# Kernel tuning notes

Measured on AMD Instinct MI355X. Metric: run time of the kernel, lower is better.

## Reference

```python
import jax, jax.numpy as jnp
import numpy as np
import math

B, T, C, D = 8, 2048, 1024, 1024
N_LAYER, LAYER_ID = 24, 12


def setup_inputs() -> dict:
    key = jax.random.key(0)
    ks = jax.random.split(key, 5)
    r01 = LAYER_ID / (N_LAYER - 1)
    r10 = 1.0 - LAYER_ID / N_LAYER
    ddd = np.arange(C, dtype=np.float64) / C                      # (C,)
    h = np.arange(D, dtype=np.float64)
    decay_speed = -5 + 8 * (h / (D - 1)) ** (0.7 + 1.3 * r01)     # time_decay init
    zigzag = ((np.arange(D) + 1) % 3 - 1) * 0.5
    time_first = np.log(0.3) + zigzag
    scale = C ** -0.5
    return {
        "x": jax.random.normal(ks[0], (B, T, C), jnp.float32),
        "time_decay": jnp.asarray(decay_speed, jnp.float32),
        "time_first": jnp.asarray(time_first, jnp.float32),
        "time_mix_k": jnp.asarray(ddd ** r10, jnp.float32),
        "time_mix_v": jnp.asarray(ddd ** r10 + 0.3 * r01, jnp.float32),
        "time_mix_r": jnp.asarray(ddd ** (0.5 * r10), jnp.float32),
        "Wk": jax.random.normal(ks[1], (D, C), jnp.float32) * scale,
        "Wv": jax.random.normal(ks[2], (D, C), jnp.float32) * scale,
        "Wr": jax.random.normal(ks[3], (D, C), jnp.float32) * scale,
        "Wo": jax.random.normal(ks[4], (C, D), jnp.float32) * scale,
    }


def _wkv(time_decay, time_first, k, v):
    # wkv_t = (e^{u+k_t} v_t + A_{t-1}) / (e^{u+k_t} + B_{t-1})
    # A_t = e^w A_{t-1} + e^{k_t} v_t ;  B_t likewise with v=1 ;  w = -exp(time_decay)
    # Exactly the math of the original conv1d-with-exp-curve trick, in O(T).
    ew = jnp.exp(-jnp.exp(time_decay))   # (D,)
    eu = jnp.exp(time_first)             # (D,)
    ek = jnp.exp(k)                      # [B,T,D]
    ekv = ek * v

    def step(carry, inp):
        a, b = carry                     # [B,D] each
        ekt, ekvt = inp                  # [B,D] each
        out = (eu * ekvt + a) / (eu * ekt + b)
        return (ew * a + ekvt, ew * b + ekt), out

    init = (jnp.zeros_like(ek[:, 0]), jnp.zeros_like(ek[:, 0]))
    xs = (jnp.swapaxes(ek, 0, 1), jnp.swapaxes(ekv, 0, 1))  # [T,B,D]
    _, out = jax.lax.scan(step, init, xs)
    return jnp.swapaxes(out, 0, 1)       # [B,T,D]


def reference(x, time_decay, time_first, time_mix_k, time_mix_v, time_mix_r, Wk, Wv, Wr, Wo):
    # time_shift: prepend zero row, drop last (ZeroPad2d((0,0,1,-1)))
    xx = jnp.pad(x, ((0, 0), (1, 0), (0, 0)))[:, :-1]
    xk = x * time_mix_k + xx * (1 - time_mix_k)
    xv = x * time_mix_v + xx * (1 - time_mix_v)
    xr = x * time_mix_r + xx * (1 - time_mix_r)
    k = jnp.einsum('btc,dc->btd', xk, Wk)
    v = jnp.einsum('btc,dc->btd', xv, Wv)
    sr = jax.nn.sigmoid(jnp.einsum('btc,dc->btd', xr, Wr))
    rwkv = sr * _wkv(time_decay, time_first, k, v)
    return jnp.einsum('btd,cd->btc', rwkv, Wo)
```

## Files before the change

### kernel.cpp

```cpp
#include <hip/hip_runtime.h>
#include <cstdint>
#include <cstddef>

#define Bb 8
#define Tt 2048
#define Cc 1024
#define Dd 1024
#define Mm (Bb*Tt)
#define CL 64
#define NCH (Tt/CL)


typedef __bf16  bf16x8  __attribute__((ext_vector_type(8)));
typedef float   floatx4 __attribute__((ext_vector_type(4)));

__device__ __forceinline__ ushort f2bf(float f) {
    unsigned u = __float_as_uint(f);
    u = (u + 0x7FFF + ((u >> 16) & 1)) >> 16;
    return (ushort)u;
}
__device__ __forceinline__ float bf2f(ushort u) {
    return __uint_as_float(((unsigned)u) << 16);
}

__device__ __forceinline__ void load_lds16(const void* g, void* l) {
    __builtin_amdgcn_global_load_lds((__attribute__((address_space(1))) void*)(g),
                                     (__attribute__((address_space(3))) void*)(l),
                                     16, 0, 0);
}

__global__ __launch_bounds__(256) void prep_mix(
        const float* __restrict__ x, const float* __restrict__ w,
        ushort* __restrict__ xm) {
    int i  = blockIdx.x * 256 + threadIdx.x;
    int cq = i & (Cc / 8 - 1);
    int m  = i >> 7;
    int t  = m & (Tt - 1);
    float4 xc0 = ((const float4*)x)[i * 2];
    float4 xc1 = ((const float4*)x)[i * 2 + 1];
    float4 xp0 = make_float4(0.f, 0.f, 0.f, 0.f);
    float4 xp1 = xp0;
    if (t != 0) {
        xp0 = ((const float4*)x)[(i - Cc / 8) * 2];
        xp1 = ((const float4*)x)[(i - Cc / 8) * 2 + 1];
    }
    float4 w0 = ((const float4*)w)[cq * 2];
    float4 w1 = ((const float4*)w)[cq * 2 + 1];
    ushort o[8];
    o[0] = f2bf(xc0.x * w0.x + xp0.x * (1.f - w0.x));
    o[1] = f2bf(xc0.y * w0.y + xp0.y * (1.f - w0.y));
    o[2] = f2bf(xc0.z * w0.z + xp0.z * (1.f - w0.z));
    o[3] = f2bf(xc0.w * w0.w + xp0.w * (1.f - w0.w));
    o[4] = f2bf(xc1.x * w1.x + xp1.x * (1.f - w1.x));
    o[5] = f2bf(xc1.y * w1.y + xp1.y * (1.f - w1.y));
    o[6] = f2bf(xc1.z * w1.z + xp1.z * (1.f - w1.z));
    o[7] = f2bf(xc1.w * w1.w + xp1.w * (1.f - w1.w));
    ((ulonglong2*)xm)[i] = *(const ulonglong2*)o;
}

__global__ __launch_bounds__(256) void cvt_w(
        const float* __restrict__ wk, const float* __restrict__ wv,
        const float* __restrict__ wr, const float* __restrict__ wo,
        ushort* __restrict__ ok, ushort* __restrict__ ov,
        ushort* __restrict__ orr, ushort* __restrict__ oo) {
    int i = blockIdx.x * 256 + threadIdx.x;
    int sel = i >> 18;
    int j = i & ((1 << 18) - 1);
    const float* s = sel == 0 ? wk : sel == 1 ? wv : sel == 2 ? wr : wo;
    ushort* d      = sel == 0 ? ok : sel == 1 ? ov : sel == 2 ? orr : oo;
    float4 f = ((const float4*)s)[j];
    ushort4 o;
    o.x = f2bf(f.x); o.y = f2bf(f.y); o.z = f2bf(f.z); o.w = f2bf(f.w);
    ((ushort4*)d)[j] = o;
}

template<int MODE>
__global__ __launch_bounds__(256) void gemm_nt(
        const ushort* __restrict__ A, const ushort* __restrict__ Bw,
        void* __restrict__ Co, int Ndim, int Kdim) {
    __shared__ __attribute__((aligned(16))) __bf16 As[128 * 32];
    __shared__ __attribute__((aligned(16))) __bf16 Bs[128 * 32];
    const int tid  = threadIdx.x;
    const int lane = tid & 63;
    const int quad = lane >> 4;
    const int fr   = lane & 15;
    const int wave = tid >> 6;
    const int wm   = (wave >> 1) * 64;
    const int wn   = (wave & 1) * 64;
    const long tm  = (long)blockIdx.x * 128;
    const long tn  = (long)blockIdx.y * 128;

    const int srow  = tid >> 2;
    const int spart = tid & 3;
    const ushort* Ag0 = A + (tm + srow) * (long)Kdim + spart * 8;
    const ushort* Ag1 = Ag0 + 64 * (long)Kdim;
    const ushort* Bg0 = Bw + (tn + srow) * (long)Kdim + spart * 8;
    const ushort* Bg1 = Bg0 + 64 * (long)Kdim;
    __bf16* AlA = &As[wave * 512];
    __bf16* AlB = &As[2048 + wave * 512];
    __bf16* BlA = &Bs[wave * 512];
    __bf16* BlB = &Bs[2048 + wave * 512];

    floatx4 zero = {0.f, 0.f, 0.f, 0.f};
    floatx4 acc[4][4];
#pragma unroll
    for (int a1 = 0; a1 < 4; a1++)
#pragma unroll
        for (int b1 = 0; b1 < 4; b1++) acc[a1][b1] = zero;

    for (int kt = 0; kt < Kdim; kt += 32) {
        __syncthreads();
        load_lds16(Ag0 + kt, AlA);
        load_lds16(Ag1 + kt, AlB);
        load_lds16(Bg0 + kt, BlA);
        load_lds16(Bg1 + kt, BlB);
        __syncthreads();

        bf16x8 af[4], bfg[4];
#pragma unroll
        for (int mi = 0; mi < 4; mi++)
            af[mi] = *(const bf16x8*)&As[(wm + mi * 16 + fr) * 32 + quad * 8];
#pragma unroll
        for (int ni = 0; ni < 4; ni++)
            bfg[ni] = *(const bf16x8*)&Bs[(wn + ni * 16 + fr) * 32 + quad * 8];
#pragma unroll
        for (int mi = 0; mi < 4; mi++)
#pragma unroll
            for (int ni = 0; ni < 4; ni++)
                acc[mi][ni] = __builtin_amdgcn_mfma_f32_16x16x32_bf16(
                    af[mi], bfg[ni], acc[mi][ni], 0, 0, 0);
    }

#pragma unroll
    for (int mi = 0; mi < 4; mi++)
#pragma unroll
        for (int ni = 0; ni < 4; ni++)
#pragma unroll
            for (int r = 0; r < 4; r++) {
                long grow = tm + wm + mi * 16 + quad * 4 + r;
                long gcol = tn + wn + ni * 16 + fr;
                float v = acc[mi][ni][r];
                if (MODE == 2) v = 1.f / (1.f + __expf(-v));
                if (MODE == 0)      ((float*)Co)[grow * Ndim + gcol] = v;
                else if (MODE == 3) ((_Float16*)Co)[grow * Ndim + gcol] = (_Float16)v;
                else                ((ushort*)Co)[grow * Ndim + gcol] = f2bf(v);
            }
}

__global__ __launch_bounds__(256) void wkv_part(
        const _Float16* __restrict__ kb, const ushort* __restrict__ vb,
        const float* __restrict__ decay,
        float* __restrict__ pa, float* __restrict__ pb) {
    int gid = blockIdx.x * 256 + threadIdx.x;
    int d = gid & (Dd - 1);
    int c = (gid >> 10) & (NCH - 1);
    int b = gid >> 15;
    float ew = __expf(-__expf(decay[d]));
    size_t base = ((size_t)b * Tt + (size_t)c * CL) * Dd + d;
    float a = 0.f, bs = 0.f;
    for (int i0 = 0; i0 < CL; i0 += 8) {
        float kr[8], vr[8];
#pragma unroll
        for (int j = 0; j < 8; j++) {
            size_t idx = base + (size_t)(i0 + j) * Dd;
            kr[j] = (float)kb[idx]; vr[j] = bf2f(vb[idx]);
        }
#pragma unroll
        for (int j = 0; j < 8; j++) {
            float ek = __expf(kr[j]);
            a  = ew * a  + ek * vr[j];
            bs = ew * bs + ek;
        }
    }
    int sidx = c * (Bb * Dd) + b * Dd + d;
    pa[sidx] = a; pb[sidx] = bs;
}

__global__ __launch_bounds__(256) void wkv_prefix(
        const float* __restrict__ pa, const float* __restrict__ pb,
        const float* __restrict__ decay,
        float* __restrict__ sa, float* __restrict__ sb) {
    int gid = blockIdx.x * 256 + threadIdx.x;
    int d = gid & (Dd - 1);
    float ewL = __expf(-__expf(decay[d]) * (float)CL);
    float ca = 0.f, cb = 0.f;
#pragma unroll
    for (int c = 0; c < NCH; c++) {
        int idx = c * (Bb * Dd) + gid;
        sa[idx] = ca; sb[idx] = cb;
        ca = ewL * ca + pa[idx];
        cb = ewL * cb + pb[idx];
    }
}

__global__ __launch_bounds__(256) void wkv_chunk(
        const _Float16* __restrict__ kb, const ushort* __restrict__ vb,
        const ushort* __restrict__ sr,
        const float* __restrict__ decay, const float* __restrict__ tf,
        const float* __restrict__ sa, const float* __restrict__ sb,
        ushort* __restrict__ rw) {
    int gid = blockIdx.x * 256 + threadIdx.x;
    int d = gid & (Dd - 1);
    int c = (gid >> 10) & (NCH - 1);
    int b = gid >> 15;
    float ew = __expf(-__expf(decay[d]));
    float eu = __expf(tf[d]);
    int sidx = c * (Bb * Dd) + b * Dd + d;
    float a = sa[sidx], bs = sb[sidx];
    size_t base = ((size_t)b * Tt + (size_t)c * CL) * Dd + d;
    for (int i0 = 0; i0 < CL; i0 += 8) {
        float kr[8], vr[8], rr[8];
#pragma unroll
        for (int j = 0; j < 8; j++) {
            size_t idx = base + (size_t)(i0 + j) * Dd;
            kr[j] = (float)kb[idx]; vr[j] = bf2f(vb[idx]); rr[j] = bf2f(sr[idx]);
        }
#pragma unroll
        for (int j = 0; j < 8; j++) {
            float ek  = __expf(kr[j]);
            float ekv = ek * vr[j];
            float out = (eu * ekv + a) / (eu * ek + bs);
            a  = ew * a  + ekv;
            bs = ew * bs + ek;
            rw[base + (size_t)(i0 + j) * Dd] = f2bf(rr[j] * out);
        }
    }
}

extern "C" void kernel_launch(void* const* d_in, const int* in_sizes, int n_in,
                              void* d_out, int out_size, void* d_ws, size_t ws_size,
                              hipStream_t stream) {
    (void)in_sizes; (void)n_in; (void)out_size; (void)ws_size;
    const float* x  = (const float*)d_in[0];
    const float* td = (const float*)d_in[1];
    const float* tf = (const float*)d_in[2];
    const float* mk = (const float*)d_in[3];
    const float* mv = (const float*)d_in[4];
    const float* mr = (const float*)d_in[5];
    const float* Wk = (const float*)d_in[6];
    const float* Wv = (const float*)d_in[7];
    const float* Wr = (const float*)d_in[8];
    const float* Wo = (const float*)d_in[9];
    float* out = (float*)d_out;

    char* p = (char*)d_ws;
    auto take = [&](size_t n) { char* r = p; p += n; return r; };
    ushort*   xb = (ushort*)take((size_t)Mm * Cc * 2);
    _Float16* kb = (_Float16*)take((size_t)Mm * Dd * 2);
    ushort*   vb = (ushort*)take((size_t)Mm * Dd * 2);
    ushort*   sb = (ushort*)take((size_t)Mm * Dd * 2);
    ushort*   wk = (ushort*)take((size_t)Dd * Cc * 2);
    ushort*   wv = (ushort*)take((size_t)Dd * Cc * 2);
    ushort*   wr = (ushort*)take((size_t)Dd * Cc * 2);
    ushort*   wo = (ushort*)take((size_t)Cc * Dd * 2);
    float*    pa = (float*)take((size_t)Bb * NCH * Dd * 4);
    float*    pb = (float*)take((size_t)Bb * NCH * Dd * 4);
    float*    sa = (float*)take((size_t)Bb * NCH * Dd * 4);
    float*    sbst = (float*)take((size_t)Bb * NCH * Dd * 4);
    ushort*   rw = xb;

    const int prep_grid = Mm * Cc / 8 / 256;
    dim3 g1(Mm / 128, Dd / 128);
    dim3 g2(Mm / 128, Cc / 128);
    const int wkv_grid = (Bb * NCH * Dd) / 256;

    cvt_w<<<4096, 256, 0, stream>>>(Wk, Wv, Wr, Wo, wk, wv, wr, wo);

    prep_mix<<<prep_grid, 256, 0, stream>>>(x, mk, xb);
    gemm_nt<3><<<g1, 256, 0, stream>>>(xb, wk, kb, Dd, Cc);

    prep_mix<<<prep_grid, 256, 0, stream>>>(x, mv, xb);
    gemm_nt<1><<<g1, 256, 0, stream>>>(xb, wv, vb, Dd, Cc);

    prep_mix<<<prep_grid, 256, 0, stream>>>(x, mr, xb);
    gemm_nt<2><<<g1, 256, 0, stream>>>(xb, wr, sb, Dd, Cc);

    wkv_part  <<<wkv_grid, 256, 0, stream>>>(kb, vb, td, pa, pb);
    wkv_prefix<<<(Bb * Dd) / 256, 256, 0, stream>>>(pa, pb, td, sa, sbst);
    wkv_chunk <<<wkv_grid, 256, 0, stream>>>(kb, vb, sb, td, tf, sa, sbst, rw);

    gemm_nt<0><<<g2, 256, 0, stream>>>(rw, wo, out, Cc, Dd);
}
```

Baseline: 443.6 us.

## Fuse three token-shift mix kernels and XOR-swizzle GEMM LDS tiles

The three separate prep_mix launches become one prep_mix3 kernel. It reads x and the previous row once and writes all three bf16 mixed inputs, which removes two extra full passes over the fp32 activations. The workspace is re-laid out so the k/v/r mixed buffers are later reused as the v, sigmoid(r) and rwkv outputs. The GEMM also XOR-permutes the 16-byte k-chunk each thread stages into LDS, and the fragment read undoes that permutation, to spread LDS bank accesses. The cost is a larger workspace and some index arithmetic.

```diff
diff --git a/kernel.cpp b/kernel.cpp
--- a/kernel.cpp
+++ b/kernel.cpp
@@ -29,33 +29,43 @@
                                      16, 0, 0);
 }
 
-__global__ __launch_bounds__(256) void prep_mix(
-        const float* __restrict__ x, const float* __restrict__ w,
-        ushort* __restrict__ xm) {
+__global__ __launch_bounds__(256) void prep_mix3(
+        const float* __restrict__ x,
+        const float* __restrict__ mk, const float* __restrict__ mv,
+        const float* __restrict__ mr,
+        ushort* __restrict__ xk, ushort* __restrict__ xv, ushort* __restrict__ xr) {
     int i  = blockIdx.x * 256 + threadIdx.x;
     int cq = i & (Cc / 8 - 1);
     int m  = i >> 7;
     int t  = m & (Tt - 1);
-    float4 xc0 = ((const float4*)x)[i * 2];
-    float4 xc1 = ((const float4*)x)[i * 2 + 1];
-    float4 xp0 = make_float4(0.f, 0.f, 0.f, 0.f);
-    float4 xp1 = xp0;
+    float xc[8], xp[8];
+    *(float4*)&xc[0] = ((const float4*)x)[i * 2];
+    *(float4*)&xc[4] = ((const float4*)x)[i * 2 + 1];
     if (t != 0) {
-        xp0 = ((const float4*)x)[(i - Cc / 8) * 2];
-        xp1 = ((const float4*)x)[(i - Cc / 8) * 2 + 1];
-    }
-    float4 w0 = ((const float4*)w)[cq * 2];
-    float4 w1 = ((const float4*)w)[cq * 2 + 1];
-    ushort o[8];
-    o[0] = f2bf(xc0.x * w0.x + xp0.x * (1.f - w0.x));
-    o[1] = f2bf(xc0.y * w0.y + xp0.y * (1.f - w0.y));
-    o[2] = f2bf(xc0.z * w0.z + xp0.z * (1.f - w0.z));
-    o[3] = f2bf(xc0.w * w0.w + xp0.w * (1.f - w0.w));
-    o[4] = f2bf(xc1.x * w1.x + xp1.x * (1.f - w1.x));
-    o[5] = f2bf(xc1.y * w1.y + xp1.y * (1.f - w1.y));
-    o[6] = f2bf(xc1.z * w1.z + xp1.z * (1.f - w1.z));
-    o[7] = f2bf(xc1.w * w1.w + xp1.w * (1.f - w1.w));
-    ((ulonglong2*)xm)[i] = *(const ulonglong2*)o;
+        *(float4*)&xp[0] = ((const float4*)x)[(i - Cc / 8) * 2];
+        *(float4*)&xp[4] = ((const float4*)x)[(i - Cc / 8) * 2 + 1];
+    } else {
+#pragma unroll
+        for (int j = 0; j < 8; j++) xp[j] = 0.f;
+    }
+    float wk[8], wv[8], wr[8];
+    *(float4*)&wk[0] = ((const float4*)mk)[cq * 2];
+    *(float4*)&wk[4] = ((const float4*)mk)[cq * 2 + 1];
+    *(float4*)&wv[0] = ((const float4*)mv)[cq * 2];
+    *(float4*)&wv[4] = ((const float4*)mv)[cq * 2 + 1];
+    *(float4*)&wr[0] = ((const float4*)mr)[cq * 2];
+    *(float4*)&wr[4] = ((const float4*)mr)[cq * 2 + 1];
+    ushort ok[8], ov[8], orr[8];
+#pragma unroll
+    for (int j = 0; j < 8; j++) {
+        float d = xc[j] - xp[j];
+        ok[j]  = f2bf(xp[j] + d * wk[j]);
+        ov[j]  = f2bf(xp[j] + d * wv[j]);
+        orr[j] = f2bf(xp[j] + d * wr[j]);
+    }
+    ((ulonglong2*)xk)[i] = *(const ulonglong2*)ok;
+    ((ulonglong2*)xv)[i] = *(const ulonglong2*)ov;
+    ((ulonglong2*)xr)[i] = *(const ulonglong2*)orr;
 }
 
 __global__ __launch_bounds__(256) void cvt_w(
@@ -91,7 +101,7 @@
     const long tn  = (long)blockIdx.y * 128;
 
     const int srow  = tid >> 2;
-    const int spart = tid & 3;
+    const int spart = (tid & 3) ^ ((tid >> 3) & 3);
     const ushort* Ag0 = A + (tm + srow) * (long)Kdim + spart * 8;
     const ushort* Ag1 = Ag0 + 64 * (long)Kdim;
     const ushort* Bg0 = Bw + (tn + srow) * (long)Kdim + spart * 8;
@@ -101,6 +111,8 @@
     __bf16* BlA = &Bs[wave * 512];
     __bf16* BlB = &Bs[2048 + wave * 512];
 
+    const int swz = (fr >> 1) & 3;
+
     floatx4 zero = {0.f, 0.f, 0.f, 0.f};
     floatx4 acc[4][4];
 #pragma unroll
@@ -119,10 +131,10 @@
         bf16x8 af[4], bfg[4];
 #pragma unroll
         for (int mi = 0; mi < 4; mi++)
-            af[mi] = *(const bf16x8*)&As[(wm + mi * 16 + fr) * 32 + quad * 8];
+            af[mi] = *(const bf16x8*)&As[(wm + mi * 16 + fr) * 32 + (quad ^ swz) * 8];
 #pragma unroll
         for (int ni = 0; ni < 4; ni++)
-            bfg[ni] = *(const bf16x8*)&Bs[(wn + ni * 16 + fr) * 32 + quad * 8];
+            bfg[ni] = *(const bf16x8*)&Bs[(wn + ni * 16 + fr) * 32 + (quad ^ swz) * 8];
 #pragma unroll
         for (int mi = 0; mi < 4; mi++)
 #pragma unroll
@@ -245,10 +257,10 @@
 
     char* p = (char*)d_ws;
     auto take = [&](size_t n) { char* r = p; p += n; return r; };
-    ushort*   xb = (ushort*)take((size_t)Mm * Cc * 2);
+    ushort*   xk = (ushort*)take((size_t)Mm * Cc * 2);
+    ushort*   xv = (ushort*)take((size_t)Mm * Cc * 2);
+    ushort*   xr = (ushort*)take((size_t)Mm * Cc * 2);
     _Float16* kb = (_Float16*)take((size_t)Mm * Dd * 2);
-    ushort*   vb = (ushort*)take((size_t)Mm * Dd * 2);
-    ushort*   sb = (ushort*)take((size_t)Mm * Dd * 2);
     ushort*   wk = (ushort*)take((size_t)Dd * Cc * 2);
     ushort*   wv = (ushort*)take((size_t)Dd * Cc * 2);
     ushort*   wr = (ushort*)take((size_t)Dd * Cc * 2);
@@ -257,23 +269,20 @@
     float*    pb = (float*)take((size_t)Bb * NCH * Dd * 4);
     float*    sa = (float*)take((size_t)Bb * NCH * Dd * 4);
     float*    sbst = (float*)take((size_t)Bb * NCH * Dd * 4);
-    ushort*   rw = xb;
-
-    const int prep_grid = Mm * Cc / 8 / 256;
+    ushort*   vb = xk;
+    ushort*   sb = xv;
+    ushort*   rw = xr;
+
     dim3 g1(Mm / 128, Dd / 128);
     dim3 g2(Mm / 128, Cc / 128);
     const int wkv_grid = (Bb * NCH * Dd) / 256;
 
     cvt_w<<<4096, 256, 0, stream>>>(Wk, Wv, Wr, Wo, wk, wv, wr, wo);
-
-    prep_mix<<<prep_grid, 256, 0, stream>>>(x, mk, xb);
-    gemm_nt<3><<<g1, 256, 0, stream>>>(xb, wk, kb, Dd, Cc);
-
-    prep_mix<<<prep_grid, 256, 0, stream>>>(x, mv, xb);
-    gemm_nt<1><<<g1, 256, 0, stream>>>(xb, wv, vb, Dd, Cc);
-
-    prep_mix<<<prep_grid, 256, 0, stream>>>(x, mr, xb);
-    gemm_nt<2><<<g1, 256, 0, stream>>>(xb, wr, sb, Dd, Cc);
+    prep_mix3<<<Mm * Cc / 8 / 256, 256, 0, stream>>>(x, mk, mv, mr, xk, xv, xr);
+
+    gemm_nt<3><<<g1, 256, 0, stream>>>(xk, wk, kb, Dd, Cc);
+    gemm_nt<1><<<g1, 256, 0, stream>>>(xv, wv, vb, Dd, Cc);
+    gemm_nt<2><<<g1, 256, 0, stream>>>(xr, wr, sb, Dd, Cc);
 
     wkv_part  <<<wkv_grid, 256, 0, stream>>>(kb, vb, td, pa, pb);
     wkv_prefix<<<(Bb * Dd) / 256, 256, 0, stream>>>(pa, pb, td, sa, sbst);
```

Measured after the change: 421.7 us. 4.9% less time.
